# Performance work log

Measured on AMD Instinct MI355X. Metric: run time of the kernel, lower is better.

## Reference

```python
import jax, jax.numpy as jnp
import numpy as np

HEADS = 8


def setup_inputs() -> dict:
    key = jax.random.key(0)
    k1, k2, k3, k4, k5, k6 = jax.random.split(key, 6)
    B, S, E = 2, 2048, 512
    D = E // HEADS
    return {
        "values": jax.random.normal(k1, (B, S, E), dtype=jnp.float32),
        "keys": jax.random.normal(k2, (B, S, E), dtype=jnp.float32),
        "queries": jax.random.normal(k3, (B, S, E), dtype=jnp.float32),
        "mask": jax.random.randint(k4, (B, 1, 1, S), 0, 2, dtype=jnp.int32),
        "W_v": jax.random.normal(k5, (D, D), dtype=jnp.float32) * (1.0 / np.sqrt(D)),
        "W_o": jax.random.normal(k6, (E, E), dtype=jnp.float32) * (1.0 / np.sqrt(E)),
        "b_o": jnp.zeros((E,), dtype=jnp.float32),
    }


def reference(values, keys, queries, mask, W_v, W_o, b_o):
    B, S, E = queries.shape
    H = HEADS
    D = E // H
    # reshape to (b, s, h, d) and apply the SAME W_v linear to v, k, q
    # (faithful to the original, which calls self.values on all three)
    v = jnp.einsum('bshd,ed->bshe', values.reshape(B, -1, H, D), W_v)
    k = jnp.einsum('bshd,ed->bshe', keys.reshape(B, -1, H, D), W_v)
    q = jnp.einsum('bshd,ed->bshe', queries.reshape(B, -1, H, D), W_v)
    # unscaled attention scores (original has no 1/sqrt(d))
    energy = jnp.einsum('bqhd,bkhd->bhqk', q, k)  # (b, h, q, k)
    energy = jnp.where(mask == 0, -jnp.inf, energy)
    attn = jax.nn.softmax(energy, axis=3)
    out = jnp.einsum('bhqk,bkhd->bqhd', attn, v)  # (b, q, h, d)
    out = out.reshape(B, S, E)
    return out @ W_o.T + b_o
```

## Files before the change

kernel.cpp:

```cpp
#include <hip/hip_runtime.h>


#define B_ 2
#define S_ 2048
#define E_ 512
#define H_ 8
#define D_ 64

#define LOG2E 1.4426950408889634f
#define KEEP_BIAS (-92.332483f)

typedef unsigned short ushort_t;
typedef __attribute__((ext_vector_type(8))) short short8;
typedef __attribute__((ext_vector_type(8))) _Float16 half8;
typedef __attribute__((ext_vector_type(4))) float f32x4;

__device__ __forceinline__ ushort_t f2bs(float x) {
    union { float f; unsigned int u; } a; a.f = x;
    unsigned int u = a.u;
    u += 0x7fffu + ((u >> 16) & 1u);
    return (ushort_t)(u >> 16);
}
__device__ __forceinline__ ushort_t f2hs(float x) {
    _Float16 h = (_Float16)x;
    ushort_t u; __builtin_memcpy(&u, &h, 2);
    return u;
}

__global__ void __launch_bounds__(256) proj_mfma(
    const float* __restrict__ quer, const float* __restrict__ keys,
    const float* __restrict__ vals, const float* __restrict__ Wv,
    const float* __restrict__ Wo,
    ushort_t* __restrict__ qf, ushort_t* __restrict__ kf,
    ushort_t* __restrict__ vt, ushort_t* __restrict__ Wob)
{
    __shared__ ushort_t As[3][64 * 72];
    __shared__ ushort_t Bs[64 * 72];
    const int bx = blockIdx.x;
    const int t = threadIdx.x;

    if (blockIdx.y == 1) {
        if (bx < 128) {
            int g = (bx * 256 + t) * 8;
            float4 f0 = *(const float4*)(Wo + g);
            float4 f1 = *(const float4*)(Wo + g + 4);
            ushort_t tmp[8] = {f2bs(f0.x), f2bs(f0.y), f2bs(f0.z), f2bs(f0.w),
                               f2bs(f1.x), f2bs(f1.y), f2bs(f1.z), f2bs(f1.w)};
            *(uint4*)&Wob[g] = *(uint4*)tmp;
        }
        return;
    }

    const int st = bx & 31, bh = bx >> 5;
    const int b = bh >> 3, h = bh & 7;
    const int s0 = st * 64;

    {
        int e = t >> 2, dg = (t & 3) * 16;
        const float4* g = (const float4*)(Wv + e * 64 + dg);
        ushort_t tmp[16];
        #pragma unroll
        for (int q = 0; q < 4; ++q) {
            float4 f = g[q];
            tmp[q * 4 + 0] = f2hs(f.x); tmp[q * 4 + 1] = f2hs(f.y);
            tmp[q * 4 + 2] = f2hs(f.z); tmp[q * 4 + 3] = f2hs(f.w);
        }
        *(uint4*)&Bs[e * 72 + dg]     = *(uint4*)tmp;
        *(uint4*)&Bs[e * 72 + dg + 8] = *(uint4*)(tmp + 8);
    }
    {
        int row = t >> 2, cg = (t & 3) * 16;
        const size_t off = ((size_t)b * S_ + s0 + row) * 512 + h * 64 + cg;
        const float* srcs[3] = {quer, keys, vals};
        #pragma unroll
        for (int tt = 0; tt < 3; ++tt) {
            const float4* g = (const float4*)(srcs[tt] + off);
            ushort_t tmp[16];
            #pragma unroll
            for (int q = 0; q < 4; ++q) {
                float4 f = g[q];
                tmp[q * 4 + 0] = f2hs(f.x); tmp[q * 4 + 1] = f2hs(f.y);
                tmp[q * 4 + 2] = f2hs(f.z); tmp[q * 4 + 3] = f2hs(f.w);
            }
            *(uint4*)&As[tt][row * 72 + cg]     = *(uint4*)tmp;
            *(uint4*)&As[tt][row * 72 + cg + 8] = *(uint4*)(tmp + 8);
        }
    }
    __syncthreads();

    const int w = t >> 6, lm = t & 15, quad = (t >> 4) & 3;

    #pragma unroll
    for (int tens = 0; tens < 3; ++tens) {
        f32x4 acc[4];
        #pragma unroll
        for (int nt = 0; nt < 4; ++nt) acc[nt] = (f32x4){0.f, 0.f, 0.f, 0.f};

        __builtin_amdgcn_s_setprio(1);
        #pragma unroll
        for (int kk = 0; kk < 2; ++kk) {
            half8 a = *(const half8*)&As[tens][(w * 16 + lm) * 72 + kk * 32 + quad * 8];
            #pragma unroll
            for (int nt = 0; nt < 4; ++nt) {
                half8 bb = *(const half8*)&Bs[(nt * 16 + lm) * 72 + kk * 32 + quad * 8];
                acc[nt] = __builtin_amdgcn_mfma_f32_16x16x32_f16(a, bb, acc[nt], 0, 0, 0);
            }
        }
        __builtin_amdgcn_s_setprio(0);

        if (tens < 2) {
            ushort_t* dst = tens == 0 ? qf : kf;
            const float sc = tens == 0 ? LOG2E : 1.0f;
            #pragma unroll
            for (int nt = 0; nt < 4; ++nt) {
                #pragma unroll
                for (int r = 0; r < 4; ++r) {
                    size_t addr = ((size_t)bh * S_ + s0 + w * 16 + quad * 4 + r) * 64 + nt * 16 + lm;
                    dst[addr] = f2hs(acc[nt][r] * sc);
                }
            }
        } else {
            #pragma unroll
            for (int nt = 0; nt < 4; ++nt) {
                unsigned int p0 = (unsigned int)f2bs(acc[nt][0]) | ((unsigned int)f2bs(acc[nt][1]) << 16);
                unsigned int p1 = (unsigned int)f2bs(acc[nt][2]) | ((unsigned int)f2bs(acc[nt][3]) << 16);
                uint2 pk; pk.x = p0; pk.y = p1;
                size_t addr = ((size_t)bh * 64 + nt * 16 + lm) * S_ + s0 + w * 16 + quad * 4;
                *(uint2*)&vt[addr] = pk;
            }
        }
    }
}

__global__ void __launch_bounds__(512, 4) attn_mfma(
    const ushort_t* __restrict__ qf, const ushort_t* __restrict__ kf,
    const ushort_t* __restrict__ vt, const int* __restrict__ mask,
    ushort_t* __restrict__ ctx)
{
    __shared__ ushort_t Ks[2][64 * 72];
    __shared__ ushort_t Vt[2][64 * 72];
    __shared__ ushort_t Ps[8 * 16 * 72];
    __shared__ float    mb[2][64];

    const int bx = blockIdx.x;
    const int qt = bx & 31;
    const int bh = bx >> 5;
    const int b  = bh >> 3;
    const int t  = threadIdx.x;
    const int w  = t >> 6;
    const int wq = w & 3;
    const int ws = w >> 2;
    const int lm = t & 15, quad = (t >> 4) & 3;
    const int q0 = qt * 64;
    const int wbase = w * 16 * 72;

    const int srow = t >> 3;
    const int scg  = (t & 7) * 8;
    const size_t kgbase = ((size_t)bh * S_ + srow) * 64 + scg;
    const size_t vgbase = ((size_t)bh * 64 + srow) * S_ + scg;

    half8 aq[2];
    {
        size_t qrow = ((size_t)bh * S_ + q0 + wq * 16 + lm) * 64 + quad * 8;
        aq[0] = *(const half8*)&qf[qrow];
        aq[1] = *(const half8*)&qf[qrow + 32];
    }
    short8 ones;
    #pragma unroll
    for (int j = 0; j < 8; ++j) ones[j] = (short)0x3F80;

    f32x4 acc[4];
    #pragma unroll
    for (int nt = 0; nt < 4; ++nt) acc[nt] = (f32x4){0.f, 0.f, 0.f, 0.f};
    f32x4 acc_l = (f32x4){0.f, 0.f, 0.f, 0.f};

    {
        *(uint4*)&Ks[0][srow * 72 + scg] = *(const uint4*)&kf[kgbase];
        *(uint4*)&Ks[1][srow * 72 + scg] = *(const uint4*)&kf[kgbase + 4096];
        *(uint4*)&Vt[0][srow * 72 + scg] = *(const uint4*)&vt[vgbase];
        *(uint4*)&Vt[1][srow * 72 + scg] = *(const uint4*)&vt[vgbase + 64];
        if (t < 128) mb[t >> 6][t & 63] = mask[b * S_ + t] ? KEEP_BIAS : -1e30f;
    }
    __syncthreads();

    for (int is = 0; is < S_ / 128; ++is) {
        const bool pf = (is + 1) < (S_ / 128);

        uint4 pk0, pk1, pv0, pv1; int mnx = 0;
        if (pf) {
            size_t ko = kgbase + (size_t)(2 * (is + 1)) * 4096;
            pk0 = *(const uint4*)&kf[ko];
            pk1 = *(const uint4*)&kf[ko + 4096];
            size_t vo = vgbase + (size_t)(2 * (is + 1)) * 64;
            pv0 = *(const uint4*)&vt[vo];
            pv1 = *(const uint4*)&vt[vo + 64];
            if (t < 128) mnx = mask[b * S_ + (2 * (is + 1)) * 64 + t];
        }

        const ushort_t* Kc = Ks[ws];
        const ushort_t* Vc = Vt[ws];

        #pragma unroll
        for (int nt = 0; nt < 4; ++nt) {
            f32x4 s = *(const f32x4*)&mb[ws][nt * 16 + quad * 4];
            __builtin_amdgcn_s_setprio(1);
            #pragma unroll
            for (int kk = 0; kk < 2; ++kk) {
                half8 ak = *(const half8*)&Kc[(nt * 16 + lm) * 72 + kk * 32 + quad * 8];
                s = __builtin_amdgcn_mfma_f32_16x16x32_f16(ak, aq[kk], s, 0, 0, 0);
            }
            __builtin_amdgcn_s_setprio(0);
            float p0 = __builtin_amdgcn_exp2f(s[0]);
            float p1 = __builtin_amdgcn_exp2f(s[1]);
            float p2 = __builtin_amdgcn_exp2f(s[2]);
            float p3 = __builtin_amdgcn_exp2f(s[3]);
            uint2 pkd;
            pkd.x = (unsigned int)f2bs(p0) | ((unsigned int)f2bs(p1) << 16);
            pkd.y = (unsigned int)f2bs(p2) | ((unsigned int)f2bs(p3) << 16);
            *(uint2*)&Ps[wbase + lm * 72 + nt * 16 + quad * 4] = pkd;
        }

        __builtin_amdgcn_s_setprio(1);
        #pragma unroll
        for (int kk = 0; kk < 2; ++kk) {
            short8 ap = *(const short8*)&Ps[wbase + lm * 72 + kk * 32 + quad * 8];
            #pragma unroll
            for (int nt = 0; nt < 4; ++nt) {
                short8 bv = *(const short8*)&Vc[(nt * 16 + lm) * 72 + kk * 32 + quad * 8];
                acc[nt] = __builtin_amdgcn_mfma_f32_16x16x32_bf16(ap, bv, acc[nt], 0, 0, 0);
            }
            acc_l = __builtin_amdgcn_mfma_f32_16x16x32_bf16(ap, ones, acc_l, 0, 0, 0);
        }
        __builtin_amdgcn_s_setprio(0);

        __syncthreads();
        if (pf) {
            *(uint4*)&Ks[0][srow * 72 + scg] = pk0;
            *(uint4*)&Ks[1][srow * 72 + scg] = pk1;
            *(uint4*)&Vt[0][srow * 72 + scg] = pv0;
            *(uint4*)&Vt[1][srow * 72 + scg] = pv1;
            if (t < 128) mb[t >> 6][t & 63] = mnx ? KEEP_BIAS : -1e30f;
            __syncthreads();
        }
    }

    float* cf = (float*)Ps;
    const int lane = t & 63;
    __syncthreads();
    if (ws == 1) {
        const int base = (wq * 64 + lane) * 18;
        #pragma unroll
        for (int nt = 0; nt < 4; ++nt) {
            #pragma unroll
            for (int r = 0; r < 4; r += 2) {
                float2 v2; v2.x = acc[nt][r]; v2.y = acc[nt][r + 1];
                *(float2*)&cf[base + nt * 4 + r] = v2;
            }
        }
    }
    __syncthreads();
    if (ws == 0) {
        const int base = (wq * 64 + lane) * 18;
        #pragma unroll
        for (int nt = 0; nt < 4; ++nt) {
            #pragma unroll
            for (int r = 0; r < 4; ++r) acc[nt][r] += cf[base + nt * 4 + r];
        }
    }
    __syncthreads();
    if (ws == 1) {
        const int base = (wq * 64 + lane) * 5;
        #pragma unroll
        for (int r = 0; r < 4; ++r) cf[base + r] = acc_l[r];
    }
    __syncthreads();

    if (ws == 0) {
        const int base = (wq * 64 + lane) * 5;
        #pragma unroll
        for (int r = 0; r < 4; ++r) acc_l[r] += cf[base + r];
        const int h = bh & 7;
        #pragma unroll
        for (int r = 0; r < 4; ++r) {
            float inv = 1.f / acc_l[r];
            int s = q0 + wq * 16 + quad * 4 + r;
            #pragma unroll
            for (int nt = 0; nt < 4; ++nt) {
                int d = nt * 16 + lm;
                ctx[((size_t)b * S_ + s) * E_ + h * D_ + d] = f2bs(acc[nt][r] * inv);
            }
        }
    }
}

__global__ void __launch_bounds__(512, 4) outproj_mfma(
    const ushort_t* __restrict__ ctx, const ushort_t* __restrict__ Wob,
    const float* __restrict__ bo, float* __restrict__ out)
{
    __shared__ ushort_t sm[4][64 * 72];
    const int m0 = blockIdx.x * 64, n0 = blockIdx.y * 64;
    const int t = threadIdx.x;
    const int w = t >> 6, wq = w & 3, wk = w >> 2;
    const int lm = t & 15, quad = (t >> 4) & 3;
    const int srow = t >> 3, scg = (t & 7) * 8;

    const size_t abase = (size_t)(m0 + srow) * E_ + scg;
    const size_t bbase = (size_t)(n0 + srow) * E_ + scg;

    f32x4 acc[4];
    #pragma unroll
    for (int nt = 0; nt < 4; ++nt) acc[nt] = (f32x4){0.f, 0.f, 0.f, 0.f};

    *(uint4*)&sm[0][srow * 72 + scg] = *(const uint4*)&ctx[abase];
    *(uint4*)&sm[1][srow * 72 + scg] = *(const uint4*)&ctx[abase + 256];
    *(uint4*)&sm[2][srow * 72 + scg] = *(const uint4*)&Wob[bbase];
    *(uint4*)&sm[3][srow * 72 + scg] = *(const uint4*)&Wob[bbase + 256];
    __syncthreads();

    const ushort_t* Ac = sm[wk];
    const ushort_t* Bc = sm[2 + wk];

    for (int is = 0; is < 4; ++is) {
        const bool pf = is < 3;
        uint4 pa0, pa1, pb0, pb1;
        if (pf) {
            pa0 = *(const uint4*)&ctx[abase + (size_t)(is + 1) * 64];
            pa1 = *(const uint4*)&ctx[abase + 256 + (size_t)(is + 1) * 64];
            pb0 = *(const uint4*)&Wob[bbase + (size_t)(is + 1) * 64];
            pb1 = *(const uint4*)&Wob[bbase + 256 + (size_t)(is + 1) * 64];
        }

        __builtin_amdgcn_s_setprio(1);
        #pragma unroll
        for (int kk = 0; kk < 2; ++kk) {
            short8 a = *(const short8*)&Ac[(wq * 16 + lm) * 72 + kk * 32 + quad * 8];
            #pragma unroll
            for (int nt = 0; nt < 4; ++nt) {
                short8 bb = *(const short8*)&Bc[(nt * 16 + lm) * 72 + kk * 32 + quad * 8];
                acc[nt] = __builtin_amdgcn_mfma_f32_16x16x32_bf16(a, bb, acc[nt], 0, 0, 0);
            }
        }
        __builtin_amdgcn_s_setprio(0);

        __syncthreads();
        if (pf) {
            *(uint4*)&sm[0][srow * 72 + scg] = pa0;
            *(uint4*)&sm[1][srow * 72 + scg] = pa1;
            *(uint4*)&sm[2][srow * 72 + scg] = pb0;
            *(uint4*)&sm[3][srow * 72 + scg] = pb1;
            __syncthreads();
        }
    }

    float* cf = (float*)sm;
    const int lane = t & 63;
    if (wk == 1) {
        const int base = (wq * 64 + lane) * 18;
        #pragma unroll
        for (int nt = 0; nt < 4; ++nt) {
            #pragma unroll
            for (int r = 0; r < 4; r += 2) {
                float2 v2; v2.x = acc[nt][r]; v2.y = acc[nt][r + 1];
                *(float2*)&cf[base + nt * 4 + r] = v2;
            }
        }
    }
    __syncthreads();
    if (wk == 0) {
        const int base = (wq * 64 + lane) * 18;
        #pragma unroll
        for (int nt = 0; nt < 4; ++nt) {
            float bias = bo[n0 + nt * 16 + lm];
            #pragma unroll
            for (int r = 0; r < 4; ++r) {
                int m = m0 + wq * 16 + quad * 4 + r;
                out[(size_t)m * E_ + n0 + nt * 16 + lm] =
                    acc[nt][r] + cf[base + nt * 4 + r] + bias;
            }
        }
    }
}

extern "C" void kernel_launch(void* const* d_in, const int* in_sizes, int n_in,
                              void* d_out, int out_size, void* d_ws, size_t ws_size,
                              hipStream_t stream) {
    const float* vals = (const float*)d_in[0];
    const float* keys = (const float*)d_in[1];
    const float* quer = (const float*)d_in[2];
    const int*   mask = (const int*)d_in[3];
    const float* Wv   = (const float*)d_in[4];
    const float* Wo   = (const float*)d_in[5];
    const float* bo   = (const float*)d_in[6];
    float* out = (float*)d_out;

    const size_t N = (size_t)B_ * H_ * S_ * D_;
    ushort_t* ws  = (ushort_t*)d_ws;
    ushort_t* qf  = ws;
    ushort_t* kf  = ws + N;
    ushort_t* vt  = ws + 2 * N;
    ushort_t* ctx = ws + 3 * N;
    ushort_t* Wob = ws + 4 * N;

    proj_mfma<<<dim3(B_ * H_ * (S_ / 64), 2), 256, 0, stream>>>(
        quer, keys, vals, Wv, Wo, qf, kf, vt, Wob);
    attn_mfma<<<B_ * H_ * (S_ / 64), 512, 0, stream>>>(qf, kf, vt, mask, ctx);
    outproj_mfma<<<dim3((B_ * S_) / 64, E_ / 64), 512, 0, stream>>>(ctx, Wob, bo, out);
}
```

Before: 126.1 us.

## Split each 64-key tile across warp halves with proper double buffering

Before, each half of the workgroup took its own 64-key tile, and the kernel did not overlap the next load with compute, since it synced, stored to LDS, then synced again. Now both halves share one 64-key tile, each taking 32 keys, and a real ping-pong buffer lets the next tile's LDS store go ahead before a single barrier per iteration. The P scratch shrinks, and the final cross-half reduction reuses the K and V buffers with fewer barriers. The cost is twice as many loop iterations, each doing half the MFMA work, so there is more barrier and loop overhead per key.

```diff
diff --git a/kernel.cpp b/kernel.cpp
--- a/kernel.cpp
+++ b/kernel.cpp
@@ -139,7 +139,7 @@
 {
     __shared__ ushort_t Ks[2][64 * 72];
     __shared__ ushort_t Vt[2][64 * 72];
-    __shared__ ushort_t Ps[8 * 16 * 72];
+    __shared__ ushort_t Ps[8][16 * 40];
     __shared__ float    mb[2][64];
 
     const int bx = blockIdx.x;
@@ -152,7 +152,6 @@
     const int ws = w >> 2;
     const int lm = t & 15, quad = (t >> 4) & 3;
     const int q0 = qt * 64;
-    const int wbase = w * 16 * 72;
 
     const int srow = t >> 3;
     const int scg  = (t & 7) * 8;
@@ -176,37 +175,32 @@
 
     {
         *(uint4*)&Ks[0][srow * 72 + scg] = *(const uint4*)&kf[kgbase];
-        *(uint4*)&Ks[1][srow * 72 + scg] = *(const uint4*)&kf[kgbase + 4096];
         *(uint4*)&Vt[0][srow * 72 + scg] = *(const uint4*)&vt[vgbase];
-        *(uint4*)&Vt[1][srow * 72 + scg] = *(const uint4*)&vt[vgbase + 64];
-        if (t < 128) mb[t >> 6][t & 63] = mask[b * S_ + t] ? KEEP_BIAS : -1e30f;
-    }
-    __syncthreads();
-
-    for (int is = 0; is < S_ / 128; ++is) {
-        const bool pf = (is + 1) < (S_ / 128);
-
-        uint4 pk0, pk1, pv0, pv1; int mnx = 0;
+        if (t < 64) mb[0][t] = mask[b * S_ + t] ? KEEP_BIAS : -1e30f;
+    }
+    __syncthreads();
+
+    for (int is = 0; is < 32; ++is) {
+        const int p = is & 1;
+        const bool pf = is < 31;
+
+        uint4 pk0, pv0; int mnx = 0;
         if (pf) {
-            size_t ko = kgbase + (size_t)(2 * (is + 1)) * 4096;
-            pk0 = *(const uint4*)&kf[ko];
-            pk1 = *(const uint4*)&kf[ko + 4096];
-            size_t vo = vgbase + (size_t)(2 * (is + 1)) * 64;
-            pv0 = *(const uint4*)&vt[vo];
-            pv1 = *(const uint4*)&vt[vo + 64];
-            if (t < 128) mnx = mask[b * S_ + (2 * (is + 1)) * 64 + t];
-        }
-
-        const ushort_t* Kc = Ks[ws];
-        const ushort_t* Vc = Vt[ws];
-
-        #pragma unroll
-        for (int nt = 0; nt < 4; ++nt) {
-            f32x4 s = *(const f32x4*)&mb[ws][nt * 16 + quad * 4];
+            pk0 = *(const uint4*)&kf[kgbase + (size_t)(is + 1) * 4096];
+            pv0 = *(const uint4*)&vt[vgbase + (size_t)(is + 1) * 64];
+            if (t < 64) mnx = mask[b * S_ + (is + 1) * 64 + t];
+        }
+
+        const ushort_t* Kc = Ks[p];
+        const ushort_t* Vc = Vt[p];
+
+        #pragma unroll
+        for (int ntk = 0; ntk < 2; ++ntk) {
+            f32x4 s = *(const f32x4*)&mb[p][ws * 32 + ntk * 16 + quad * 4];
             __builtin_amdgcn_s_setprio(1);
             #pragma unroll
             for (int kk = 0; kk < 2; ++kk) {
-                half8 ak = *(const half8*)&Kc[(nt * 16 + lm) * 72 + kk * 32 + quad * 8];
+                half8 ak = *(const half8*)&Kc[(ws * 32 + ntk * 16 + lm) * 72 + kk * 32 + quad * 8];
                 s = __builtin_amdgcn_mfma_f32_16x16x32_f16(ak, aq[kk], s, 0, 0, 0);
             }
             __builtin_amdgcn_s_setprio(0);
@@ -217,77 +211,56 @@
             uint2 pkd;
             pkd.x = (unsigned int)f2bs(p0) | ((unsigned int)f2bs(p1) << 16);
             pkd.y = (unsigned int)f2bs(p2) | ((unsigned int)f2bs(p3) << 16);
-            *(uint2*)&Ps[wbase + lm * 72 + nt * 16 + quad * 4] = pkd;
+            *(uint2*)&Ps[w][lm * 40 + ntk * 16 + quad * 4] = pkd;
         }
 
         __builtin_amdgcn_s_setprio(1);
-        #pragma unroll
-        for (int kk = 0; kk < 2; ++kk) {
-            short8 ap = *(const short8*)&Ps[wbase + lm * 72 + kk * 32 + quad * 8];
-            #pragma unroll
-            for (int nt = 0; nt < 4; ++nt) {
-                short8 bv = *(const short8*)&Vc[(nt * 16 + lm) * 72 + kk * 32 + quad * 8];
+        {
+            short8 ap = *(const short8*)&Ps[w][lm * 40 + quad * 8];
+            #pragma unroll
+            for (int nt = 0; nt < 4; ++nt) {
+                short8 bv = *(const short8*)&Vc[(nt * 16 + lm) * 72 + ws * 32 + quad * 8];
                 acc[nt] = __builtin_amdgcn_mfma_f32_16x16x32_bf16(ap, bv, acc[nt], 0, 0, 0);
             }
             acc_l = __builtin_amdgcn_mfma_f32_16x16x32_bf16(ap, ones, acc_l, 0, 0, 0);
         }
         __builtin_amdgcn_s_setprio(0);
 
+        if (pf) {
+            *(uint4*)&Ks[p ^ 1][srow * 72 + scg] = pk0;
+            *(uint4*)&Vt[p ^ 1][srow * 72 + scg] = pv0;
+            if (t < 64) mb[p ^ 1][t] = mnx ? KEEP_BIAS : -1e30f;
+        }
         __syncthreads();
-        if (pf) {
-            *(uint4*)&Ks[0][srow * 72 + scg] = pk0;
-            *(uint4*)&Ks[1][srow * 72 + scg] = pk1;
-            *(uint4*)&Vt[0][srow * 72 + scg] = pv0;
-            *(uint4*)&Vt[1][srow * 72 + scg] = pv1;
-            if (t < 128) mb[t >> 6][t & 63] = mnx ? KEEP_BIAS : -1e30f;
-            __syncthreads();
-        }
-    }
-
-    float* cf = (float*)Ps;
+    }
+
+    float* cfO = (float*)Ks;
+    float* cfL = (float*)Vt;
     const int lane = t & 63;
-    __syncthreads();
     if (ws == 1) {
-        const int base = (wq * 64 + lane) * 18;
-        #pragma unroll
-        for (int nt = 0; nt < 4; ++nt) {
-            #pragma unroll
-            for (int r = 0; r < 4; r += 2) {
-                float2 v2; v2.x = acc[nt][r]; v2.y = acc[nt][r + 1];
-                *(float2*)&cf[base + nt * 4 + r] = v2;
-            }
-        }
+        const int bO = (wq * 64 + lane) * 17;
+        const int bL = (wq * 64 + lane) * 5;
+        #pragma unroll
+        for (int nt = 0; nt < 4; ++nt)
+            #pragma unroll
+            for (int r = 0; r < 4; ++r) cfO[bO + nt * 4 + r] = acc[nt][r];
+        #pragma unroll
+        for (int r = 0; r < 4; ++r) cfL[bL + r] = acc_l[r];
     }
     __syncthreads();
     if (ws == 0) {
-        const int base = (wq * 64 + lane) * 18;
-        #pragma unroll
-        for (int nt = 0; nt < 4; ++nt) {
-            #pragma unroll
-            for (int r = 0; r < 4; ++r) acc[nt][r] += cf[base + nt * 4 + r];
-        }
-    }
-    __syncthreads();
-    if (ws == 1) {
-        const int base = (wq * 64 + lane) * 5;
-        #pragma unroll
-        for (int r = 0; r < 4; ++r) cf[base + r] = acc_l[r];
-    }
-    __syncthreads();
-
-    if (ws == 0) {
-        const int base = (wq * 64 + lane) * 5;
-        #pragma unroll
-        for (int r = 0; r < 4; ++r) acc_l[r] += cf[base + r];
+        const int bO = (wq * 64 + lane) * 17;
+        const int bL = (wq * 64 + lane) * 5;
         const int h = bh & 7;
         #pragma unroll
         for (int r = 0; r < 4; ++r) {
-            float inv = 1.f / acc_l[r];
+            float l = acc_l[r] + cfL[bL + r];
+            float inv = 1.f / l;
             int s = q0 + wq * 16 + quad * 4 + r;
             #pragma unroll
             for (int nt = 0; nt < 4; ++nt) {
-                int d = nt * 16 + lm;
-                ctx[((size_t)b * S_ + s) * E_ + h * D_ + d] = f2bs(acc[nt][r] * inv);
+                float o = acc[nt][r] + cfO[bO + nt * 4 + r];
+                ctx[((size_t)b * S_ + s) * E_ + h * D_ + nt * 16 + lm] = f2bs(o * inv);
             }
         }
     }
```

After: 126.7 us. About the same (+0.5%).

## Split attention key range across two blocks and combine partials

Applied to the files above, without the earlier changes.

The attention kernel now runs a second grid dimension that divides the 2048 keys into two halves. Each block writes unnormalised fp32 output partials and row sums to workspace. A new combine kernel adds the two halves, normalises, and writes bf16 context. Because softmax uses a fixed bias instead of a running max, the partials can simply be added. This doubles the block count so more of the GPU is busy. In exchange it adds an extra launch and about 16MB of fp32 partial traffic, and it relies on the workspace being large enough.

```diff
diff --git a/kernel.cpp b/kernel.cpp
--- a/kernel.cpp
+++ b/kernel.cpp
@@ -135,7 +135,7 @@
 __global__ void __launch_bounds__(512, 4) attn_mfma(
     const ushort_t* __restrict__ qf, const ushort_t* __restrict__ kf,
     const ushort_t* __restrict__ vt, const int* __restrict__ mask,
-    ushort_t* __restrict__ ctx)
+    float* __restrict__ Opart, float* __restrict__ lpart)
 {
     __shared__ ushort_t Ks[2][64 * 72];
     __shared__ ushort_t Vt[2][64 * 72];
@@ -143,6 +143,7 @@
     __shared__ float    mb[2][64];
 
     const int bx = blockIdx.x;
+    const int sp = blockIdx.y;
     const int qt = bx & 31;
     const int bh = bx >> 5;
     const int b  = bh >> 3;
@@ -156,8 +157,9 @@
 
     const int srow = t >> 3;
     const int scg  = (t & 7) * 8;
-    const size_t kgbase = ((size_t)bh * S_ + srow) * 64 + scg;
-    const size_t vgbase = ((size_t)bh * 64 + srow) * S_ + scg;
+    const size_t kgbase = ((size_t)bh * S_ + sp * 1024 + srow) * 64 + scg;
+    const size_t vgbase = ((size_t)bh * 64 + srow) * S_ + sp * 1024 + scg;
+    const int mbase = b * S_ + sp * 1024;
 
     half8 aq[2];
     {
@@ -179,12 +181,12 @@
         *(uint4*)&Ks[1][srow * 72 + scg] = *(const uint4*)&kf[kgbase + 4096];
         *(uint4*)&Vt[0][srow * 72 + scg] = *(const uint4*)&vt[vgbase];
         *(uint4*)&Vt[1][srow * 72 + scg] = *(const uint4*)&vt[vgbase + 64];
-        if (t < 128) mb[t >> 6][t & 63] = mask[b * S_ + t] ? KEEP_BIAS : -1e30f;
-    }
-    __syncthreads();
-
-    for (int is = 0; is < S_ / 128; ++is) {
-        const bool pf = (is + 1) < (S_ / 128);
+        if (t < 128) mb[t >> 6][t & 63] = mask[mbase + t] ? KEEP_BIAS : -1e30f;
+    }
+    __syncthreads();
+
+    for (int is = 0; is < 8; ++is) {
+        const bool pf = is < 7;
 
         uint4 pk0, pk1, pv0, pv1; int mnx = 0;
         if (pf) {
@@ -194,7 +196,7 @@
             size_t vo = vgbase + (size_t)(2 * (is + 1)) * 64;
             pv0 = *(const uint4*)&vt[vo];
             pv1 = *(const uint4*)&vt[vo + 64];
-            if (t < 128) mnx = mask[b * S_ + (2 * (is + 1)) * 64 + t];
+            if (t < 128) mnx = mask[mbase + (2 * (is + 1)) * 64 + t];
         }
 
         const ushort_t* Kc = Ks[ws];
@@ -279,18 +281,47 @@
         const int base = (wq * 64 + lane) * 5;
         #pragma unroll
         for (int r = 0; r < 4; ++r) acc_l[r] += cf[base + r];
-        const int h = bh & 7;
+        float* Op = Opart + (size_t)(sp * 512 + bx) * 4096;
+        float* Lp = lpart + (size_t)(sp * 512 + bx) * 64;
         #pragma unroll
         for (int r = 0; r < 4; ++r) {
-            float inv = 1.f / acc_l[r];
-            int s = q0 + wq * 16 + quad * 4 + r;
-            #pragma unroll
-            for (int nt = 0; nt < 4; ++nt) {
-                int d = nt * 16 + lm;
-                ctx[((size_t)b * S_ + s) * E_ + h * D_ + d] = f2bs(acc[nt][r] * inv);
-            }
-        }
-    }
+            const int qrow = wq * 16 + quad * 4 + r;
+            if (lm == 0) Lp[qrow] = acc_l[r];
+            #pragma unroll
+            for (int nt = 0; nt < 4; ++nt)
+                Op[qrow * 64 + nt * 16 + lm] = acc[nt][r];
+        }
+    }
+}
+
+__global__ void __launch_bounds__(256) combine_ctx(
+    const float* __restrict__ Opart, const float* __restrict__ lpart,
+    ushort_t* __restrict__ ctx)
+{
+    const int bx = blockIdx.x;
+    const int bh = bx >> 5, qt = bx & 31;
+    const int b = bh >> 3, h = bh & 7;
+    const int t = threadIdx.x;
+    const int row = t >> 2, cg = (t & 3) * 16;
+
+    const float* o0 = Opart + (size_t)bx * 4096 + row * 64 + cg;
+    const float* o1 = Opart + (size_t)(512 + bx) * 4096 + row * 64 + cg;
+    const float inv = 1.f / (lpart[(size_t)bx * 64 + row] +
+                             lpart[(size_t)(512 + bx) * 64 + row]);
+    ushort_t tmp[16];
+    #pragma unroll
+    for (int q = 0; q < 4; ++q) {
+        float4 a = *(const float4*)(o0 + 4 * q);
+        float4 c = *(const float4*)(o1 + 4 * q);
+        tmp[4 * q + 0] = f2bs((a.x + c.x) * inv);
+        tmp[4 * q + 1] = f2bs((a.y + c.y) * inv);
+        tmp[4 * q + 2] = f2bs((a.z + c.z) * inv);
+        tmp[4 * q + 3] = f2bs((a.w + c.w) * inv);
+    }
+    const int s = qt * 64 + row;
+    ushort_t* dst = ctx + ((size_t)b * S_ + s) * E_ + h * D_ + cg;
+    *(uint4*)dst       = *(uint4*)tmp;
+    *(uint4*)(dst + 8) = *(uint4*)(tmp + 8);
 }
 
 __global__ void __launch_bounds__(512, 4) outproj_mfma(
@@ -400,9 +431,13 @@
     ushort_t* vt  = ws + 2 * N;
     ushort_t* ctx = ws + 3 * N;
     ushort_t* Wob = ws + 4 * N;
+    float* Opart  = (float*)(ws + 4 * N + 512 * 512);
+    float* lpart  = Opart + (size_t)2 * 512 * 4096;
 
     proj_mfma<<<dim3(B_ * H_ * (S_ / 64), 2), 256, 0, stream>>>(
         quer, keys, vals, Wv, Wo, qf, kf, vt, Wob);
-    attn_mfma<<<B_ * H_ * (S_ / 64), 512, 0, stream>>>(qf, kf, vt, mask, ctx);
+    attn_mfma<<<dim3(B_ * H_ * (S_ / 64), 2), 512, 0, stream>>>(
+        qf, kf, vt, mask, Opart, lpart);
+    combine_ctx<<<B_ * H_ * (S_ / 64), 256, 0, stream>>>(Opart, lpart, ctx);
     outproj_mfma<<<dim3((B_ * S_) / 64, E_ / 64), 512, 0, stream>>>(ctx, Wob, bo, out);
 }
```

New measurement: 132.6 us. 5.2% more time.
